# Optimization experiments

Hardware: AMD Instinct MI355X
Metric: run time of the kernel (lower is better)

## Reference

```python
import jax, jax.numpy as jnp
import numpy as np

NUM_HEADS = 8


def setup_inputs() -> dict:
    key = jax.random.key(0)
    kx, k1, k2, k3, k4 = jax.random.split(key, 5)
    B, C, H, W = 32, 512, 32, 32
    x = jax.random.normal(kx, (B, C, H, W), dtype=jnp.float32)
    # Linear params (jax convention: y = x @ W + b)
    W_qkv = jax.random.normal(k1, (C, 3 * C), dtype=jnp.float32) * 0.02
    b_qkv = jax.random.normal(k2, (3 * C,), dtype=jnp.float32) * 0.02
    W_proj = jax.random.normal(k3, (C, C), dtype=jnp.float32) * 0.02
    b_proj = jax.random.normal(k4, (C,), dtype=jnp.float32) * 0.02
    return {"x": x, "W_qkv": W_qkv, "b_qkv": b_qkv, "W_proj": W_proj, "b_proj": b_proj}


def reference(x, W_qkv, b_qkv, W_proj, b_proj):
    B, C, H, W = x.shape
    hd = C // NUM_HEADS
    # flatten(2).transpose(1,2): (B, N, C), N = H*W
    xt = x.reshape(B, C, H * W).transpose(0, 2, 1)
    qkv = (xt @ W_qkv + b_qkv).reshape(B, -1, 3, NUM_HEADS, hd)
    q = qkv[:, :, 0]                      # (B, N, heads, hd)
    k = qkv[:, :, 1].mean(axis=2, keepdims=True)  # mean over HEAD axis -> (B, N, 1, hd)
    v = qkv[:, :, 2].mean(axis=2, keepdims=True)  # (B, N, 1, hd)
    scale = float(C) ** 0.5
    # attn: (B, N, heads, 1) -- batched over tokens, per the original code
    attn = jnp.einsum('bnhd,bnkd->bnhk', q, k) / scale
    attn = jax.nn.softmax(attn, axis=-1)  # size-1 axis -> ones (faithful)
    out = jnp.einsum('bnhk,bnkd->bnhd', attn, v)  # (B, N, heads, hd)
    # transpose(1,2).reshape(B,-1,C): head-first flattening, as in the original
    out = out.transpose(0, 2, 1, 3).reshape(B, -1, C)
    out = out @ W_proj + b_proj
    out = out.transpose(0, 2, 1).reshape(B, C, H, W)
    return out
```

## Files before the change

kernel.cpp:

```cpp
#include <hip/hip_runtime.h>
#include <hip/hip_bf16.h>


typedef unsigned int u32;
typedef __attribute__((ext_vector_type(8))) short short8;
typedef __attribute__((ext_vector_type(4))) float f32x4;

__device__ __forceinline__ void gll16(const void* g, void* l) {
  __builtin_amdgcn_global_load_lds(
      (const __attribute__((address_space(1))) u32*)g,
      (__attribute__((address_space(3))) u32*)l, 16, 0, 0);
}
__device__ __forceinline__ u32 packbf2(float a, float b) {
  __hip_bfloat162 p = __float22bfloat162_rn(make_float2(a, b));
  return *(u32*)&p;
}

__global__ __launch_bounds__(256) void prep_kernel(
    const float* __restrict__ Wqkv, const float* __restrict__ bqkv,
    const float* __restrict__ Wproj, __hip_bfloat16* __restrict__ Wvt,
    float* __restrict__ bv, __hip_bfloat16* __restrict__ Wpt) {
  const int bid = blockIdx.x, t = (int)threadIdx.x;
  if (bid < 256) {
    __shared__ float Tl[32][33];
    const int tr = bid >> 4, tc = bid & 15;
    const int c0 = tr * 32, p0 = tc * 32;
    const int r = t >> 5, col = t & 31;
#pragma unroll
    for (int a = 0; a < 4; ++a)
      Tl[r + a * 8][col] = Wproj[(size_t)(c0 + r + a * 8) * 512 + p0 + col];
    __syncthreads();
#pragma unroll
    for (int a = 0; a < 4; ++a)
      Wpt[(size_t)(p0 + r + a * 8) * 512 + c0 + col] = __float2bfloat16(Tl[col][r + a * 8]);
  } else {
    const int g = (bid - 256) * 256 + t;
    const int c = g >> 6, d = g & 63;
    float s = 0.f;
#pragma unroll
    for (int h = 0; h < 8; ++h) s += Wqkv[(size_t)c * 1536 + 1024 + h * 64 + d];
    Wvt[(size_t)d * 512 + c] = __float2bfloat16(s * 0.125f);
    if (g < 64) {
      float sb = 0.f;
#pragma unroll
      for (int h = 0; h < 8; ++h) sb += bqkv[1024 + h * 64 + d];
      bv[d] = sb * 0.125f;
    }
  }
}

__global__ __launch_bounds__(256) void gemm1_kernel(
    const float* __restrict__ x, const __hip_bfloat16* __restrict__ Wvt,
    const float* __restrict__ bv, __hip_bfloat16* __restrict__ V) {
  __shared__ __hip_bfloat16 Xl[2][4096];
  __shared__ __hip_bfloat16 Wl[2][4096];
  const int nt = blockIdx.x, b = blockIdx.y;
  const int t = (int)threadIdx.x, w = t >> 6, lane = t & 63;
  const int wr = w >> 1, wc = w & 1;
  const int cq = t >> 4, nq = t & 15;
  const float* xg = x + (size_t)b * 524288 + (size_t)nt * 64 + nq * 4;

  float4 xr[4];
#define XLOAD(kc)                                                            \
  do {                                                                       \
    _Pragma("unroll") for (int r = 0; r < 4; ++r)                            \
        xr[r] = *(const float4*)(xg + (size_t)((kc) * 64 + cq * 4 + r) * 1024); \
  } while (0)
#define XWRITE(buf)                                                          \
  do {                                                                       \
    _Pragma("unroll") for (int jn = 0; jn < 4; ++jn) {                       \
      int n = nq * 4 + jn;                                                   \
      u32 lo = packbf2(((const float*)&xr[0])[jn], ((const float*)&xr[1])[jn]); \
      u32 hi = packbf2(((const float*)&xr[2])[jn], ((const float*)&xr[3])[jn]); \
      int byte = (n * 128 + cq * 8) ^ (((n >> 1) & 7) << 4);                 \
      *(uint2*)((char*)&Xl[buf][0] + byte) = make_uint2(lo, hi);             \
    }                                                                        \
  } while (0)
#define WSTAGE(buf, kc)                                                      \
  do {                                                                       \
    _Pragma("unroll") for (int q = 0; q < 2; ++q) {                          \
      int g = w * 128 + q * 64 + lane;                                       \
      int r = g >> 3, ww = g & 7;                                            \
      gll16(Wvt + (size_t)r * 512 + (kc) * 64 + ((ww ^ (r & 7)) << 3),       \
            (char*)&Wl[buf][0] + (w * 128 + q * 64) * 16);                   \
    }                                                                        \
  } while (0)

  f32x4 acc[2][2] = {{{0.f, 0.f, 0.f, 0.f}, {0.f, 0.f, 0.f, 0.f}},
                     {{0.f, 0.f, 0.f, 0.f}, {0.f, 0.f, 0.f, 0.f}}};
  XLOAD(0);
  WSTAGE(0, 0);
  XWRITE(0);
  __syncthreads();
  for (int kc = 0; kc < 8; ++kc) {
    const int cur = kc & 1;
    if (kc < 7) {
      XLOAD(kc + 1);
      WSTAGE(cur ^ 1, kc + 1);
    }
    const char* Xb = (const char*)&Xl[cur][0];
    const char* Wb = (const char*)&Wl[cur][0];
#pragma unroll
    for (int kb = 0; kb < 2; ++kb) {
      short8 af[2], bf[2];
#pragma unroll
      for (int mi = 0; mi < 2; ++mi) {
        int n = wr * 32 + mi * 16 + (lane & 15);
        int gc = (kb * 4 + (lane >> 4)) ^ ((n >> 1) & 7);
        af[mi] = *(const short8*)(Xb + n * 128 + gc * 16);
      }
#pragma unroll
      for (int ni = 0; ni < 2; ++ni) {
        int d = wc * 32 + ni * 16 + (lane & 15);
        int gc = (kb * 4 + (lane >> 4)) ^ (d & 7);
        bf[ni] = *(const short8*)(Wb + d * 128 + gc * 16);
      }
#pragma unroll
      for (int mi = 0; mi < 2; ++mi)
#pragma unroll
        for (int ni = 0; ni < 2; ++ni)
          acc[mi][ni] = __builtin_amdgcn_mfma_f32_16x16x32_bf16(af[mi], bf[ni], acc[mi][ni], 0, 0, 0);
    }
    if (kc < 7) XWRITE(cur ^ 1);
    __syncthreads();
  }
#undef XLOAD
#undef XWRITE
#undef WSTAGE
#pragma unroll
  for (int ni = 0; ni < 2; ++ni) {
    const int d = wc * 32 + ni * 16 + (lane & 15);
    const float bvd = bv[d];
#pragma unroll
    for (int mi = 0; mi < 2; ++mi) {
      const int n0 = nt * 64 + wr * 32 + mi * 16 + (lane >> 4) * 4;
#pragma unroll
      for (int r = 0; r < 4; ++r)
        V[((size_t)b * 1024 + n0 + r) * 64 + d] = __float2bfloat16(acc[mi][ni][r] + bvd);
    }
  }
}

__global__ __launch_bounds__(256) void gemm2_kernel(
    const __hip_bfloat16* __restrict__ Vb, const __hip_bfloat16* __restrict__ Wpt,
    const float* __restrict__ bproj, float* __restrict__ out) {
  __shared__ char smem[32768];
  char* Zl0 = smem;
  char* Wl0 = smem + 16384;
  const int lin = (((int)blockIdx.x & 7) << 6) | ((int)blockIdx.x >> 3);
  const int ct = lin & 7, jt = (lin >> 3) & 1, b = lin >> 4;
  const int t = (int)threadIdx.x, w = t >> 6, lane = t & 63;
  const int wr = w >> 1, wc = w & 1;
  const __hip_bfloat16* Zg = Vb + (size_t)b * 65536 + (size_t)jt * 64 * 512;
  const __hip_bfloat16* Wg = Wpt + (size_t)ct * 64 * 512;

#define STAGE(buf, kc)                                                       \
  do {                                                                       \
    _Pragma("unroll") for (int q = 0; q < 2; ++q) {                          \
      int g = w * 128 + q * 64 + lane;                                       \
      int r = g >> 3, ww = g & 7;                                            \
      int cof = (kc) * 64 + ((ww ^ (r & 7)) << 3);                           \
      int ldsoff = (w * 128 + q * 64) * 16;                                  \
      gll16(Zg + (size_t)r * 512 + cof, Zl0 + (buf) * 8192 + ldsoff);        \
      gll16(Wg + (size_t)r * 512 + cof, Wl0 + (buf) * 8192 + ldsoff);        \
    }                                                                        \
  } while (0)

  f32x4 acc[2][2] = {{{0.f, 0.f, 0.f, 0.f}, {0.f, 0.f, 0.f, 0.f}},
                     {{0.f, 0.f, 0.f, 0.f}, {0.f, 0.f, 0.f, 0.f}}};
  STAGE(0, 0);
  __syncthreads();
  for (int kc = 0; kc < 8; ++kc) {
    const int cur = kc & 1;
    if (kc < 7) STAGE(cur ^ 1, kc + 1);
    const char* Zb = Zl0 + cur * 8192;
    const char* Wb = Wl0 + cur * 8192;
#pragma unroll
    for (int kb = 0; kb < 2; ++kb) {
      short8 af[2], bf[2];
#pragma unroll
      for (int mi = 0; mi < 2; ++mi) {
        int j = wr * 32 + mi * 16 + (lane & 15);
        int gc = (kb * 4 + (lane >> 4)) ^ (j & 7);
        af[mi] = *(const short8*)(Zb + j * 128 + gc * 16);
      }
#pragma unroll
      for (int ni = 0; ni < 2; ++ni) {
        int p = wc * 32 + ni * 16 + (lane & 15);
        int gc = (kb * 4 + (lane >> 4)) ^ (p & 7);
        bf[ni] = *(const short8*)(Wb + p * 128 + gc * 16);
      }
#pragma unroll
      for (int mi = 0; mi < 2; ++mi)
#pragma unroll
        for (int ni = 0; ni < 2; ++ni)
          acc[mi][ni] = __builtin_amdgcn_mfma_f32_16x16x32_bf16(af[mi], bf[ni], acc[mi][ni], 0, 0, 0);
    }
    __syncthreads();
  }
#undef STAGE
  float* Pl = (float*)smem;
#pragma unroll
  for (int ni = 0; ni < 2; ++ni) {
    const int p = wc * 32 + ni * 16 + (lane & 15);
    const float bp = bproj[ct * 64 + p];
#pragma unroll
    for (int mi = 0; mi < 2; ++mi) {
      const int j0 = wr * 32 + mi * 16 + (lane >> 4) * 4;
#pragma unroll
      for (int r = 0; r < 4; ++r) Pl[(j0 + r) * 65 + p] = acc[mi][ni][r] + bp;
    }
  }
  __syncthreads();
  float* ob = out + ((size_t)b * 512 + ct * 64) * 1024 + jt * 64;
#pragma unroll 8
  for (int k = 0; k < 32; ++k) {
    int F = t + 256 * k;
    int cl = F >> 7;
    int rem = F & 127;
    int rep = rem >> 4;
    int j4 = (rem & 15) * 4;
    float4 v;
    v.x = Pl[(j4 + 0) * 65 + cl];
    v.y = Pl[(j4 + 1) * 65 + cl];
    v.z = Pl[(j4 + 2) * 65 + cl];
    v.w = Pl[(j4 + 3) * 65 + cl];
    *(float4*)(ob + (size_t)cl * 1024 + rep * 128 + j4) = v;
  }
}

extern "C" void kernel_launch(void* const* d_in, const int* in_sizes, int n_in,
                              void* d_out, int out_size, void* d_ws, size_t ws_size,
                              hipStream_t stream) {
  (void)in_sizes; (void)n_in; (void)out_size; (void)ws_size;
  const float* x     = (const float*)d_in[0];
  const float* Wqkv  = (const float*)d_in[1];
  const float* bqkv  = (const float*)d_in[2];
  const float* Wproj = (const float*)d_in[3];
  const float* bproj = (const float*)d_in[4];
  float* out = (float*)d_out;
  char* ws = (char*)d_ws;
  __hip_bfloat16* Wvt = (__hip_bfloat16*)(ws);
  __hip_bfloat16* Wpt = (__hip_bfloat16*)(ws + 65536);
  float*          bv  = (float*)(ws + 589824);
  __hip_bfloat16* Vb  = (__hip_bfloat16*)(ws + 590080);

  prep_kernel<<<384, 256, 0, stream>>>(Wqkv, bqkv, Wproj, Wvt, bv, Wpt);
  gemm1_kernel<<<dim3(16, 32), 256, 0, stream>>>(x, Wvt, bv, Vb);
  gemm2_kernel<<<512, 256, 0, stream>>>(Vb, Wpt, bproj, out);
}
```

Baseline: 142.8 us.

## Load MFMA fragments directly from global memory, dropping LDS staging in both GEMMs

Both GEMM kernels stop staging tiles through LDS with barriers. Each lane now loads its MFMA operand fragments straight from global memory into registers, double-buffered in registers. In gemm1 the fp32 x values are read as strided scalar loads and packed to bf16 per lane. This removes LDS traffic and __syncthreads, but gives up cross-wave reuse of tiles, so each wave reloads shared operands. The x loads in gemm1 are also uncoalesced in the k direction, which increases global and L2 traffic.

```diff
diff --git a/kernel.cpp b/kernel.cpp
--- a/kernel.cpp
+++ b/kernel.cpp
@@ -6,11 +6,8 @@
 typedef __attribute__((ext_vector_type(8))) short short8;
 typedef __attribute__((ext_vector_type(4))) float f32x4;
 
-__device__ __forceinline__ void gll16(const void* g, void* l) {
-  __builtin_amdgcn_global_load_lds(
-      (const __attribute__((address_space(1))) u32*)g,
-      (__attribute__((address_space(3))) u32*)l, 16, 0, 0);
-}
+union FragU { u32 u[4]; short8 s; };
+
 __device__ __forceinline__ u32 packbf2(float a, float b) {
   __hip_bfloat162 p = __float22bfloat162_rn(make_float2(a, b));
   return *(u32*)&p;
@@ -52,88 +49,60 @@
 __global__ __launch_bounds__(256) void gemm1_kernel(
     const float* __restrict__ x, const __hip_bfloat16* __restrict__ Wvt,
     const float* __restrict__ bv, __hip_bfloat16* __restrict__ V) {
-  __shared__ __hip_bfloat16 Xl[2][4096];
-  __shared__ __hip_bfloat16 Wl[2][4096];
   const int nt = blockIdx.x, b = blockIdx.y;
   const int t = (int)threadIdx.x, w = t >> 6, lane = t & 63;
   const int wr = w >> 1, wc = w & 1;
-  const int cq = t >> 4, nq = t & 15;
-  const float* xg = x + (size_t)b * 524288 + (size_t)nt * 64 + nq * 4;
-
-  float4 xr[4];
-#define XLOAD(kc)                                                            \
-  do {                                                                       \
-    _Pragma("unroll") for (int r = 0; r < 4; ++r)                            \
-        xr[r] = *(const float4*)(xg + (size_t)((kc) * 64 + cq * 4 + r) * 1024); \
-  } while (0)
-#define XWRITE(buf)                                                          \
-  do {                                                                       \
-    _Pragma("unroll") for (int jn = 0; jn < 4; ++jn) {                       \
-      int n = nq * 4 + jn;                                                   \
-      u32 lo = packbf2(((const float*)&xr[0])[jn], ((const float*)&xr[1])[jn]); \
-      u32 hi = packbf2(((const float*)&xr[2])[jn], ((const float*)&xr[3])[jn]); \
-      int byte = (n * 128 + cq * 8) ^ (((n >> 1) & 7) << 4);                 \
-      *(uint2*)((char*)&Xl[buf][0] + byte) = make_uint2(lo, hi);             \
-    }                                                                        \
-  } while (0)
-#define WSTAGE(buf, kc)                                                      \
-  do {                                                                       \
-    _Pragma("unroll") for (int q = 0; q < 2; ++q) {                          \
-      int g = w * 128 + q * 64 + lane;                                       \
-      int r = g >> 3, ww = g & 7;                                            \
-      gll16(Wvt + (size_t)r * 512 + (kc) * 64 + ((ww ^ (r & 7)) << 3),       \
-            (char*)&Wl[buf][0] + (w * 128 + q * 64) * 16);                   \
-    }                                                                        \
-  } while (0)
-
+  const int lr = lane & 15, ko = lane >> 4;
+  const float* xg = x + (size_t)b * 524288 + (size_t)(ko * 8) * 1024 + nt * 64 + wr * 32 + lr;
+  const __hip_bfloat16* wg = Wvt + (size_t)(wc * 32 + lr) * 512 + ko * 8;
+
+  float xv0[2][8], xv1[2][8];
+  short8 br0[2], br1[2];
   f32x4 acc[2][2] = {{{0.f, 0.f, 0.f, 0.f}, {0.f, 0.f, 0.f, 0.f}},
                      {{0.f, 0.f, 0.f, 0.f}, {0.f, 0.f, 0.f, 0.f}}};
-  XLOAD(0);
-  WSTAGE(0, 0);
-  XWRITE(0);
-  __syncthreads();
-  for (int kc = 0; kc < 8; ++kc) {
-    const int cur = kc & 1;
-    if (kc < 7) {
-      XLOAD(kc + 1);
-      WSTAGE(cur ^ 1, kc + 1);
-    }
-    const char* Xb = (const char*)&Xl[cur][0];
-    const char* Wb = (const char*)&Wl[cur][0];
-#pragma unroll
-    for (int kb = 0; kb < 2; ++kb) {
-      short8 af[2], bf[2];
-#pragma unroll
-      for (int mi = 0; mi < 2; ++mi) {
-        int n = wr * 32 + mi * 16 + (lane & 15);
-        int gc = (kb * 4 + (lane >> 4)) ^ ((n >> 1) & 7);
-        af[mi] = *(const short8*)(Xb + n * 128 + gc * 16);
-      }
-#pragma unroll
-      for (int ni = 0; ni < 2; ++ni) {
-        int d = wc * 32 + ni * 16 + (lane & 15);
-        int gc = (kb * 4 + (lane >> 4)) ^ (d & 7);
-        bf[ni] = *(const short8*)(Wb + d * 128 + gc * 16);
-      }
-#pragma unroll
-      for (int mi = 0; mi < 2; ++mi)
-#pragma unroll
-        for (int ni = 0; ni < 2; ++ni)
-          acc[mi][ni] = __builtin_amdgcn_mfma_f32_16x16x32_bf16(af[mi], bf[ni], acc[mi][ni], 0, 0, 0);
-    }
-    if (kc < 7) XWRITE(cur ^ 1);
-    __syncthreads();
-  }
-#undef XLOAD
-#undef XWRITE
-#undef WSTAGE
+
+#define LX(dst, kc)                                                   \
+  do {                                                                \
+    _Pragma("unroll") for (int mi = 0; mi < 2; ++mi)                  \
+    _Pragma("unroll") for (int j = 0; j < 8; ++j)                     \
+        dst[mi][j] = xg[(size_t)((kc) + j) * 1024 + mi * 16];         \
+  } while (0)
+#define LB(dst, kc)                                                   \
+  do {                                                                \
+    _Pragma("unroll") for (int ni = 0; ni < 2; ++ni)                  \
+        dst[ni] = *(const short8*)(wg + ni * 8192 + (kc));            \
+  } while (0)
+#define CMP1(xv, br)                                                  \
+  do {                                                                \
+    _Pragma("unroll") for (int mi = 0; mi < 2; ++mi) {                \
+      FragU f;                                                        \
+      _Pragma("unroll") for (int p = 0; p < 4; ++p)                   \
+          f.u[p] = packbf2(xv[mi][2 * p], xv[mi][2 * p + 1]);         \
+      _Pragma("unroll") for (int ni = 0; ni < 2; ++ni)                \
+          acc[mi][ni] = __builtin_amdgcn_mfma_f32_16x16x32_bf16(      \
+              f.s, br[ni], acc[mi][ni], 0, 0, 0);                     \
+    }                                                                 \
+  } while (0)
+
+  LX(xv0, 0);  LB(br0, 0);
+  LX(xv1, 32); LB(br1, 32);
+  for (int kc = 0; kc < 512; kc += 64) {
+    CMP1(xv0, br0);
+    if (kc < 448) { LX(xv0, kc + 64); LB(br0, kc + 64); }
+    CMP1(xv1, br1);
+    if (kc < 448) { LX(xv1, kc + 96); LB(br1, kc + 96); }
+  }
+#undef LX
+#undef LB
+#undef CMP1
+
 #pragma unroll
   for (int ni = 0; ni < 2; ++ni) {
-    const int d = wc * 32 + ni * 16 + (lane & 15);
+    const int d = wc * 32 + ni * 16 + lr;
     const float bvd = bv[d];
 #pragma unroll
     for (int mi = 0; mi < 2; ++mi) {
-      const int n0 = nt * 64 + wr * 32 + mi * 16 + (lane >> 4) * 4;
+      const int n0 = nt * 64 + wr * 32 + mi * 16 + ko * 4;
 #pragma unroll
       for (int r = 0; r < 4; ++r)
         V[((size_t)b * 1024 + n0 + r) * 64 + d] = __float2bfloat16(acc[mi][ni][r] + bvd);
@@ -144,69 +113,56 @@
 __global__ __launch_bounds__(256) void gemm2_kernel(
     const __hip_bfloat16* __restrict__ Vb, const __hip_bfloat16* __restrict__ Wpt,
     const float* __restrict__ bproj, float* __restrict__ out) {
-  __shared__ char smem[32768];
-  char* Zl0 = smem;
-  char* Wl0 = smem + 16384;
+  __shared__ float Pl[64 * 65];
   const int lin = (((int)blockIdx.x & 7) << 6) | ((int)blockIdx.x >> 3);
   const int ct = lin & 7, jt = (lin >> 3) & 1, b = lin >> 4;
   const int t = (int)threadIdx.x, w = t >> 6, lane = t & 63;
   const int wr = w >> 1, wc = w & 1;
-  const __hip_bfloat16* Zg = Vb + (size_t)b * 65536 + (size_t)jt * 64 * 512;
-  const __hip_bfloat16* Wg = Wpt + (size_t)ct * 64 * 512;
-
-#define STAGE(buf, kc)                                                       \
-  do {                                                                       \
-    _Pragma("unroll") for (int q = 0; q < 2; ++q) {                          \
-      int g = w * 128 + q * 64 + lane;                                       \
-      int r = g >> 3, ww = g & 7;                                            \
-      int cof = (kc) * 64 + ((ww ^ (r & 7)) << 3);                           \
-      int ldsoff = (w * 128 + q * 64) * 16;                                  \
-      gll16(Zg + (size_t)r * 512 + cof, Zl0 + (buf) * 8192 + ldsoff);        \
-      gll16(Wg + (size_t)r * 512 + cof, Wl0 + (buf) * 8192 + ldsoff);        \
-    }                                                                        \
-  } while (0)
-
+  const int lr = lane & 15, ko = lane >> 4;
+  const __hip_bfloat16* zg = Vb + (size_t)b * 65536 + (size_t)(jt * 64 + wr * 32 + lr) * 512 + ko * 8;
+  const __hip_bfloat16* wg = Wpt + (size_t)(ct * 64 + wc * 32 + lr) * 512 + ko * 8;
+
+  short8 za0[2], za1[2], wb0[2], wb1[2];
   f32x4 acc[2][2] = {{{0.f, 0.f, 0.f, 0.f}, {0.f, 0.f, 0.f, 0.f}},
                      {{0.f, 0.f, 0.f, 0.f}, {0.f, 0.f, 0.f, 0.f}}};
-  STAGE(0, 0);
-  __syncthreads();
-  for (int kc = 0; kc < 8; ++kc) {
-    const int cur = kc & 1;
-    if (kc < 7) STAGE(cur ^ 1, kc + 1);
-    const char* Zb = Zl0 + cur * 8192;
-    const char* Wb = Wl0 + cur * 8192;
-#pragma unroll
-    for (int kb = 0; kb < 2; ++kb) {
-      short8 af[2], bf[2];
-#pragma unroll
-      for (int mi = 0; mi < 2; ++mi) {
-        int j = wr * 32 + mi * 16 + (lane & 15);
-        int gc = (kb * 4 + (lane >> 4)) ^ (j & 7);
-        af[mi] = *(const short8*)(Zb + j * 128 + gc * 16);
-      }
-#pragma unroll
-      for (int ni = 0; ni < 2; ++ni) {
-        int p = wc * 32 + ni * 16 + (lane & 15);
-        int gc = (kb * 4 + (lane >> 4)) ^ (p & 7);
-        bf[ni] = *(const short8*)(Wb + p * 128 + gc * 16);
-      }
-#pragma unroll
-      for (int mi = 0; mi < 2; ++mi)
-#pragma unroll
-        for (int ni = 0; ni < 2; ++ni)
-          acc[mi][ni] = __builtin_amdgcn_mfma_f32_16x16x32_bf16(af[mi], bf[ni], acc[mi][ni], 0, 0, 0);
-    }
-    __syncthreads();
-  }
-#undef STAGE
-  float* Pl = (float*)smem;
+
+#define LZ(dst, kc)                                                   \
+  do {                                                                \
+    _Pragma("unroll") for (int mi = 0; mi < 2; ++mi)                  \
+        dst[mi] = *(const short8*)(zg + mi * 8192 + (kc));            \
+  } while (0)
+#define LW(dst, kc)                                                   \
+  do {                                                                \
+    _Pragma("unroll") for (int ni = 0; ni < 2; ++ni)                  \
+        dst[ni] = *(const short8*)(wg + ni * 8192 + (kc));            \
+  } while (0)
+#define CMP2(za, wb)                                                  \
+  do {                                                                \
+    _Pragma("unroll") for (int mi = 0; mi < 2; ++mi)                  \
+    _Pragma("unroll") for (int ni = 0; ni < 2; ++ni)                  \
+        acc[mi][ni] = __builtin_amdgcn_mfma_f32_16x16x32_bf16(        \
+            za[mi], wb[ni], acc[mi][ni], 0, 0, 0);                    \
+  } while (0)
+
+  LZ(za0, 0);  LW(wb0, 0);
+  LZ(za1, 32); LW(wb1, 32);
+  for (int kc = 0; kc < 512; kc += 64) {
+    CMP2(za0, wb0);
+    if (kc < 448) { LZ(za0, kc + 64); LW(wb0, kc + 64); }
+    CMP2(za1, wb1);
+    if (kc < 448) { LZ(za1, kc + 96); LW(wb1, kc + 96); }
+  }
+#undef LZ
+#undef LW
+#undef CMP2
+
 #pragma unroll
   for (int ni = 0; ni < 2; ++ni) {
-    const int p = wc * 32 + ni * 16 + (lane & 15);
+    const int p = wc * 32 + ni * 16 + lr;
     const float bp = bproj[ct * 64 + p];
 #pragma unroll
     for (int mi = 0; mi < 2; ++mi) {
-      const int j0 = wr * 32 + mi * 16 + (lane >> 4) * 4;
+      const int j0 = wr * 32 + mi * 16 + ko * 4;
 #pragma unroll
       for (int r = 0; r < 4; ++r) Pl[(j0 + r) * 65 + p] = acc[mi][ni][r] + bp;
     }
```

Result: slower. 163.4 us (+14.5%).

## Halve GEMM tile rows to double block count in both GEMM kernels

Applied to the files above, without the earlier changes.

Both GEMM kernels now use 32-row output tiles instead of 64, with each of the four waves computing a 32x16 slice, so the launch grids double to 1024 blocks. The x load and LDS layout in gemm1 are reorganised for the narrower tile, and the gemm2 block remapping and output transpose are adjusted to match. The aim is more blocks in flight and more latency hiding on a memory-bound problem. In exchange, each block reuses the weight tile over fewer rows, and the MFMA-to-load ratio per wave drops.

```diff
diff --git a/kernel.cpp b/kernel.cpp
--- a/kernel.cpp
+++ b/kernel.cpp
@@ -52,42 +52,41 @@
 __global__ __launch_bounds__(256) void gemm1_kernel(
     const float* __restrict__ x, const __hip_bfloat16* __restrict__ Wvt,
     const float* __restrict__ bv, __hip_bfloat16* __restrict__ V) {
-  __shared__ __hip_bfloat16 Xl[2][4096];
-  __shared__ __hip_bfloat16 Wl[2][4096];
+  __shared__ char smem[24576];
+  char* Xl0 = smem;
+  char* Wl0 = smem + 8192;
   const int nt = blockIdx.x, b = blockIdx.y;
   const int t = (int)threadIdx.x, w = t >> 6, lane = t & 63;
-  const int wr = w >> 1, wc = w & 1;
-  const int cq = t >> 4, nq = t & 15;
-  const float* xg = x + (size_t)b * 524288 + (size_t)nt * 64 + nq * 4;
-
-  float4 xr[4];
-#define XLOAD(kc)                                                            \
-  do {                                                                       \
-    _Pragma("unroll") for (int r = 0; r < 4; ++r)                            \
-        xr[r] = *(const float4*)(xg + (size_t)((kc) * 64 + cq * 4 + r) * 1024); \
-  } while (0)
-#define XWRITE(buf)                                                          \
-  do {                                                                       \
-    _Pragma("unroll") for (int jn = 0; jn < 4; ++jn) {                       \
-      int n = nq * 4 + jn;                                                   \
-      u32 lo = packbf2(((const float*)&xr[0])[jn], ((const float*)&xr[1])[jn]); \
-      u32 hi = packbf2(((const float*)&xr[2])[jn], ((const float*)&xr[3])[jn]); \
-      int byte = (n * 128 + cq * 8) ^ (((n >> 1) & 7) << 4);                 \
-      *(uint2*)((char*)&Xl[buf][0] + byte) = make_uint2(lo, hi);             \
-    }                                                                        \
-  } while (0)
-#define WSTAGE(buf, kc)                                                      \
-  do {                                                                       \
-    _Pragma("unroll") for (int q = 0; q < 2; ++q) {                          \
-      int g = w * 128 + q * 64 + lane;                                       \
-      int r = g >> 3, ww = g & 7;                                            \
-      gll16(Wvt + (size_t)r * 512 + (kc) * 64 + ((ww ^ (r & 7)) << 3),       \
-            (char*)&Wl[buf][0] + (w * 128 + q * 64) * 16);                   \
-    }                                                                        \
-  } while (0)
-
-  f32x4 acc[2][2] = {{{0.f, 0.f, 0.f, 0.f}, {0.f, 0.f, 0.f, 0.f}},
-                     {{0.f, 0.f, 0.f, 0.f}, {0.f, 0.f, 0.f, 0.f}}};
+  const int lr = lane & 15, ko = lane >> 4;
+  const int cq = t >> 3, nq = t & 7;
+  const float* xg = x + (size_t)b * 524288 + (size_t)(cq * 2) * 1024 + nt * 32 + nq * 4;
+
+  float4 xr0, xr1;
+  f32x4 acc[2] = {{0.f, 0.f, 0.f, 0.f}, {0.f, 0.f, 0.f, 0.f}};
+
+#define XLOAD(kc)                                                      \
+  do {                                                                 \
+    xr0 = *(const float4*)(xg + (size_t)(kc) * 65536);                 \
+    xr1 = *(const float4*)(xg + (size_t)(kc) * 65536 + 1024);          \
+  } while (0)
+#define XWRITE(buf)                                                    \
+  do {                                                                 \
+    _Pragma("unroll") for (int j = 0; j < 4; ++j) {                    \
+      int n = nq * 4 + j;                                              \
+      u32 pv = packbf2(((const float*)&xr0)[j], ((const float*)&xr1)[j]); \
+      *(u32*)(Xl0 + (buf) * 4096 + ((n * 128 + cq * 4) ^ ((n & 7) << 4))) = pv; \
+    }                                                                  \
+  } while (0)
+#define WSTAGE(buf, kc)                                                \
+  do {                                                                 \
+    _Pragma("unroll") for (int q = 0; q < 2; ++q) {                    \
+      int g = t + 256 * q;                                             \
+      int r = g >> 3, ww = g & 7;                                      \
+      gll16(Wvt + (size_t)r * 512 + (kc) * 64 + ((ww ^ (r & 7)) << 3), \
+            Wl0 + (buf) * 8192 + g * 16);                              \
+    }                                                                  \
+  } while (0)
+
   XLOAD(0);
   WSTAGE(0, 0);
   XWRITE(0);
@@ -98,28 +97,23 @@
       XLOAD(kc + 1);
       WSTAGE(cur ^ 1, kc + 1);
     }
-    const char* Xb = (const char*)&Xl[cur][0];
-    const char* Wb = (const char*)&Wl[cur][0];
+    const char* Xb = Xl0 + cur * 4096;
+    const char* Wb = Wl0 + cur * 8192;
 #pragma unroll
     for (int kb = 0; kb < 2; ++kb) {
-      short8 af[2], bf[2];
+      short8 af[2], bfr;
 #pragma unroll
       for (int mi = 0; mi < 2; ++mi) {
-        int n = wr * 32 + mi * 16 + (lane & 15);
-        int gc = (kb * 4 + (lane >> 4)) ^ ((n >> 1) & 7);
-        af[mi] = *(const short8*)(Xb + n * 128 + gc * 16);
-      }
-#pragma unroll
-      for (int ni = 0; ni < 2; ++ni) {
-        int d = wc * 32 + ni * 16 + (lane & 15);
-        int gc = (kb * 4 + (lane >> 4)) ^ (d & 7);
-        bf[ni] = *(const short8*)(Wb + d * 128 + gc * 16);
+        int n = mi * 16 + lr;
+        af[mi] = *(const short8*)(Xb + ((n * 128 + kb * 64 + ko * 16) ^ ((n & 7) << 4)));
+      }
+      {
+        int d = w * 16 + lr;
+        bfr = *(const short8*)(Wb + d * 128 + (((kb * 4 + ko) ^ (d & 7)) << 4));
       }
 #pragma unroll
       for (int mi = 0; mi < 2; ++mi)
-#pragma unroll
-        for (int ni = 0; ni < 2; ++ni)
-          acc[mi][ni] = __builtin_amdgcn_mfma_f32_16x16x32_bf16(af[mi], bf[ni], acc[mi][ni], 0, 0, 0);
+        acc[mi] = __builtin_amdgcn_mfma_f32_16x16x32_bf16(af[mi], bfr, acc[mi], 0, 0, 0);
     }
     if (kc < 7) XWRITE(cur ^ 1);
     __syncthreads();
@@ -127,99 +121,94 @@
 #undef XLOAD
 #undef XWRITE
 #undef WSTAGE
-#pragma unroll
-  for (int ni = 0; ni < 2; ++ni) {
-    const int d = wc * 32 + ni * 16 + (lane & 15);
-    const float bvd = bv[d];
-#pragma unroll
-    for (int mi = 0; mi < 2; ++mi) {
-      const int n0 = nt * 64 + wr * 32 + mi * 16 + (lane >> 4) * 4;
-#pragma unroll
-      for (int r = 0; r < 4; ++r)
-        V[((size_t)b * 1024 + n0 + r) * 64 + d] = __float2bfloat16(acc[mi][ni][r] + bvd);
-    }
+
+  const int d = w * 16 + lr;
+  const float bvd = bv[d];
+#pragma unroll
+  for (int mi = 0; mi < 2; ++mi) {
+    const int n0 = nt * 32 + mi * 16 + ko * 4;
+#pragma unroll
+    for (int r = 0; r < 4; ++r)
+      V[((size_t)b * 1024 + n0 + r) * 64 + d] = __float2bfloat16(acc[mi][r] + bvd);
   }
 }
 
 __global__ __launch_bounds__(256) void gemm2_kernel(
     const __hip_bfloat16* __restrict__ Vb, const __hip_bfloat16* __restrict__ Wpt,
     const float* __restrict__ bproj, float* __restrict__ out) {
-  __shared__ char smem[32768];
+  __shared__ char smem[24576];
   char* Zl0 = smem;
-  char* Wl0 = smem + 16384;
-  const int lin = (((int)blockIdx.x & 7) << 6) | ((int)blockIdx.x >> 3);
-  const int ct = lin & 7, jt = (lin >> 3) & 1, b = lin >> 4;
+  char* Wl0 = smem + 8192;
+  const int bid = (int)blockIdx.x;
+  const int lin = ((bid & 7) << 7) | (bid >> 3);
+  const int ct = lin & 7, jt = (lin >> 3) & 3, b = lin >> 5;
   const int t = (int)threadIdx.x, w = t >> 6, lane = t & 63;
-  const int wr = w >> 1, wc = w & 1;
-  const __hip_bfloat16* Zg = Vb + (size_t)b * 65536 + (size_t)jt * 64 * 512;
-  const __hip_bfloat16* Wg = Wpt + (size_t)ct * 64 * 512;
-
-#define STAGE(buf, kc)                                                       \
-  do {                                                                       \
-    _Pragma("unroll") for (int q = 0; q < 2; ++q) {                          \
-      int g = w * 128 + q * 64 + lane;                                       \
-      int r = g >> 3, ww = g & 7;                                            \
-      int cof = (kc) * 64 + ((ww ^ (r & 7)) << 3);                           \
-      int ldsoff = (w * 128 + q * 64) * 16;                                  \
-      gll16(Zg + (size_t)r * 512 + cof, Zl0 + (buf) * 8192 + ldsoff);        \
-      gll16(Wg + (size_t)r * 512 + cof, Wl0 + (buf) * 8192 + ldsoff);        \
-    }                                                                        \
-  } while (0)
-
-  f32x4 acc[2][2] = {{{0.f, 0.f, 0.f, 0.f}, {0.f, 0.f, 0.f, 0.f}},
-                     {{0.f, 0.f, 0.f, 0.f}, {0.f, 0.f, 0.f, 0.f}}};
+  const int lr = lane & 15, ko = lane >> 4;
+  const __hip_bfloat16* Zg = Vb + (size_t)b * 65536 + (size_t)(jt * 32) * 512;
+  const __hip_bfloat16* Wg = Wpt + (size_t)(ct * 64) * 512;
+
+#define STAGE(buf, kc)                                                 \
+  do {                                                                 \
+    {                                                                  \
+      int g = t;                                                       \
+      int r = g >> 3, ww = g & 7;                                      \
+      gll16(Zg + (size_t)r * 512 + (kc) * 64 + ((ww ^ (r & 7)) << 3),  \
+            Zl0 + (buf) * 4096 + g * 16);                              \
+    }                                                                  \
+    _Pragma("unroll") for (int q = 0; q < 2; ++q) {                    \
+      int g = t + 256 * q;                                             \
+      int r = g >> 3, ww = g & 7;                                      \
+      gll16(Wg + (size_t)r * 512 + (kc) * 64 + ((ww ^ (r & 7)) << 3),  \
+            Wl0 + (buf) * 8192 + g * 16);                              \
+    }                                                                  \
+  } while (0)
+
+  f32x4 acc[2] = {{0.f, 0.f, 0.f, 0.f}, {0.f, 0.f, 0.f, 0.f}};
   STAGE(0, 0);
   __syncthreads();
   for (int kc = 0; kc < 8; ++kc) {
     const int cur = kc & 1;
     if (kc < 7) STAGE(cur ^ 1, kc + 1);
-    const char* Zb = Zl0 + cur * 8192;
+    const char* Zb = Zl0 + cur * 4096;
     const char* Wb = Wl0 + cur * 8192;
 #pragma unroll
     for (int kb = 0; kb < 2; ++kb) {
-      short8 af[2], bf[2];
+      short8 af[2], bfr;
 #pragma unroll
       for (int mi = 0; mi < 2; ++mi) {
-        int j = wr * 32 + mi * 16 + (lane & 15);
-        int gc = (kb * 4 + (lane >> 4)) ^ (j & 7);
-        af[mi] = *(const short8*)(Zb + j * 128 + gc * 16);
-      }
-#pragma unroll
-      for (int ni = 0; ni < 2; ++ni) {
-        int p = wc * 32 + ni * 16 + (lane & 15);
-        int gc = (kb * 4 + (lane >> 4)) ^ (p & 7);
-        bf[ni] = *(const short8*)(Wb + p * 128 + gc * 16);
+        int j = mi * 16 + lr;
+        af[mi] = *(const short8*)(Zb + j * 128 + (((kb * 4 + ko) ^ (j & 7)) << 4));
+      }
+      {
+        int p = w * 16 + lr;
+        bfr = *(const short8*)(Wb + p * 128 + (((kb * 4 + ko) ^ (p & 7)) << 4));
       }
 #pragma unroll
       for (int mi = 0; mi < 2; ++mi)
-#pragma unroll
-        for (int ni = 0; ni < 2; ++ni)
-          acc[mi][ni] = __builtin_amdgcn_mfma_f32_16x16x32_bf16(af[mi], bf[ni], acc[mi][ni], 0, 0, 0);
+        acc[mi] = __builtin_amdgcn_mfma_f32_16x16x32_bf16(af[mi], bfr, acc[mi], 0, 0, 0);
     }
     __syncthreads();
   }
 #undef STAGE
+
   float* Pl = (float*)smem;
-#pragma unroll
-  for (int ni = 0; ni < 2; ++ni) {
-    const int p = wc * 32 + ni * 16 + (lane & 15);
-    const float bp = bproj[ct * 64 + p];
-#pragma unroll
-    for (int mi = 0; mi < 2; ++mi) {
-      const int j0 = wr * 32 + mi * 16 + (lane >> 4) * 4;
-#pragma unroll
-      for (int r = 0; r < 4; ++r) Pl[(j0 + r) * 65 + p] = acc[mi][ni][r] + bp;
-    }
+  const int p = w * 16 + lr;
+  const float bp = bproj[ct * 64 + p];
+#pragma unroll
+  for (int mi = 0; mi < 2; ++mi) {
+#pragma unroll
+    for (int r = 0; r < 4; ++r)
+      Pl[(mi * 16 + ko * 4 + r) * 65 + p] = acc[mi][r] + bp;
   }
   __syncthreads();
-  float* ob = out + ((size_t)b * 512 + ct * 64) * 1024 + jt * 64;
-#pragma unroll 8
-  for (int k = 0; k < 32; ++k) {
+  float* ob = out + ((size_t)b * 512 + ct * 64) * 1024 + jt * 32;
+#pragma unroll
+  for (int k = 0; k < 16; ++k) {
     int F = t + 256 * k;
-    int cl = F >> 7;
-    int rem = F & 127;
-    int rep = rem >> 4;
-    int j4 = (rem & 15) * 4;
+    int cl = F >> 6;
+    int rem = F & 63;
+    int rep = rem >> 3;
+    int j4 = (rem & 7) * 4;
     float4 v;
     v.x = Pl[(j4 + 0) * 65 + cl];
     v.y = Pl[(j4 + 1) * 65 + cl];
@@ -246,6 +235,6 @@
   __hip_bfloat16* Vb  = (__hip_bfloat16*)(ws + 590080);
 
   prep_kernel<<<384, 256, 0, stream>>>(Wqkv, bqkv, Wproj, Wvt, bv, Wpt);
-  gemm1_kernel<<<dim3(16, 32), 256, 0, stream>>>(x, Wvt, bv, Vb);
-  gemm2_kernel<<<512, 256, 0, stream>>>(Vb, Wpt, bproj, out);
-}
+  gemm1_kernel<<<dim3(32, 32), 256, 0, stream>>>(x, Wvt, bv, Vb);
+  gemm2_kernel<<<1024, 256, 0, stream>>>(Vb, Wpt, bproj, out);
+}
```

Result: faster. 133.1 us (-6.8%).
